# Optimization experiments

Hardware: AMD Instinct MI355X
Metric: run time of the kernel (lower is better)

Reference implementation:

```python
import jax, jax.numpy as jnp
import numpy as np

B, N, IN_DIM, HID = 8, 2048, 128, 64
LN_EPS = 1e-5
NEG_INF = -9e15
LRELU_SLOPE = 0.2


def setup_inputs() -> dict:
    key = jax.random.key(0)
    k1, k2, k3, k4, k5, k6 = jax.random.split(key, 6)
    stdv = 1.0 / np.sqrt(HID)
    adj = jax.random.randint(k1, (B, N, N), 0, 2, dtype=jnp.int32)
    # ensure self-loops so every row has at least one valid entry
    adj = adj.at[:, jnp.arange(N), jnp.arange(N)].set(1)
    return {
        "adj": adj,
        "x": jax.random.normal(k2, (B, N, IN_DIM), dtype=jnp.float32),
        "h": jax.random.normal(k3, (B, N, HID), dtype=jnp.float32),
        "X2H": jax.random.uniform(k4, (IN_DIM, 3 * HID), minval=-stdv, maxval=stdv, dtype=jnp.float32),
        "H2H": jax.random.uniform(k5, (HID, 3 * HID), minval=-stdv, maxval=stdv, dtype=jnp.float32),
        "a": jax.random.uniform(k6, (2 * HID, 1), minval=-stdv, maxval=stdv, dtype=jnp.float32),
    }


def _gated_inputs(x, h, X2H, H2H):
    gate_x = x @ X2H          # [B,N,3H]
    gate_h = h @ H2H          # [B,N,3H]
    i_r, i_i, i_n = jnp.split(gate_x, 3, axis=2)
    h_r, h_i, h_n = jnp.split(gate_h, 3, axis=2)
    resetgate = jax.nn.sigmoid(i_r + h_r)
    inputgate = jax.nn.sigmoid(i_i + h_i)
    irh = i_n + resetgate * h_n
    mu = jnp.mean(irh, axis=-1, keepdims=True)
    var = jnp.mean(jnp.square(irh - mu), axis=-1, keepdims=True)
    irh = (irh - mu) * jax.lax.rsqrt(var + LN_EPS)  # layer_norm, no affine
    newgate = jnp.tanh(irh)
    return newgate + inputgate * (h - newgate)


def reference(adj, x, h, X2H, H2H, a):
    Wh = _gated_inputs(x, h, X2H, H2H)              # [B,N,H]
    Wh1 = Wh @ a[:HID]                              # [B,N,1]
    Wh2 = Wh @ a[HID:]                              # [B,N,1]
    e = jax.nn.leaky_relu(Wh1 + jnp.swapaxes(Wh2, 1, 2), LRELU_SLOPE)  # [B,N,N]
    scores = jnp.where(adj != 0, e, jnp.float32(NEG_INF))
    attention = jax.nn.softmax(scores, axis=2)
    h_prime = attention @ Wh                        # [B,N,H]
    return (h_prime, Wh)
```

## Files before the change

kernel.cpp:

```cpp
#include <hip/hip_runtime.h>

constexpr int BB  = 8;
constexpr int NN  = 2048;
constexpr int IND = 128;
constexpr int HD  = 64;
constexpr float LN_EPS = 1e-5f;
constexpr float SLOPE  = 0.2f;

typedef _Float16 half8 __attribute__((ext_vector_type(8)));
typedef _Float16 half4 __attribute__((ext_vector_type(4)));
typedef float    f32x4 __attribute__((ext_vector_type(4)));

__device__ __forceinline__ float wave_sum(float v) {
    #pragma unroll
    for (int off = 32; off > 0; off >>= 1) v += __shfl_xor(v, off);
    return v;
}
__device__ __forceinline__ float wave_max(float v) {
    #pragma unroll
    for (int off = 32; off > 0; off >>= 1) v = fmaxf(v, __shfl_xor(v, off));
    return v;
}

__global__ __launch_bounds__(256) void k_gates(
    const float* __restrict__ x, const float* __restrict__ h,
    const float* __restrict__ X2H, const float* __restrict__ H2H,
    const float* __restrict__ a,
    float* __restrict__ Wh_out, _Float16* __restrict__ Whh2,
    float* __restrict__ Wh1, float* __restrict__ Wh2)
{
    const int lane = threadIdx.x & 63;
    const int wid  = threadIdx.x >> 6;
    const int base = (blockIdx.x * 4 + wid) * 8;

    float gx0[8] = {0}, gx1[8] = {0}, gx2[8] = {0};
    float gh0[8] = {0}, gh1[8] = {0}, gh2[8] = {0};

    for (int d4 = 0; d4 < IND; d4 += 4) {
        float w0[4], w1[4], w2[4];
        #pragma unroll
        for (int dd = 0; dd < 4; ++dd) {
            const float* wp = X2H + (size_t)(d4 + dd) * 192;
            w0[dd] = wp[lane]; w1[dd] = wp[64 + lane]; w2[dd] = wp[128 + lane];
        }
        #pragma unroll
        for (int rr = 0; rr < 8; ++rr) {
            f32x4 xv = *(const f32x4*)(x + (size_t)(base + rr) * IND + d4);
            #pragma unroll
            for (int dd = 0; dd < 4; ++dd) {
                gx0[rr] = fmaf(xv[dd], w0[dd], gx0[rr]);
                gx1[rr] = fmaf(xv[dd], w1[dd], gx1[rr]);
                gx2[rr] = fmaf(xv[dd], w2[dd], gx2[rr]);
            }
        }
    }
    for (int d4 = 0; d4 < HD; d4 += 4) {
        float w0[4], w1[4], w2[4];
        #pragma unroll
        for (int dd = 0; dd < 4; ++dd) {
            const float* wp = H2H + (size_t)(d4 + dd) * 192;
            w0[dd] = wp[lane]; w1[dd] = wp[64 + lane]; w2[dd] = wp[128 + lane];
        }
        #pragma unroll
        for (int rr = 0; rr < 8; ++rr) {
            f32x4 hv = *(const f32x4*)(h + (size_t)(base + rr) * HD + d4);
            #pragma unroll
            for (int dd = 0; dd < 4; ++dd) {
                gh0[rr] = fmaf(hv[dd], w0[dd], gh0[rr]);
                gh1[rr] = fmaf(hv[dd], w1[dd], gh1[rr]);
                gh2[rr] = fmaf(hv[dd], w2[dd], gh2[rr]);
            }
        }
    }

    const float a0 = a[lane], a1 = a[64 + lane];
    half8 p8;
    for (int rr = 0; rr < 8; ++rr) {
        const int row = base + rr;
        const float hr = h[(size_t)row * HD + lane];
        const float rg = 1.f / (1.f + __expf(-(gx0[rr] + gh0[rr])));
        const float ig = 1.f / (1.f + __expf(-(gx1[rr] + gh1[rr])));
        float irh = gx2[rr] + rg * gh2[rr];
        const float mu = wave_sum(irh) * (1.f / 64.f);
        const float dv = irh - mu;
        const float var = wave_sum(dv * dv) * (1.f / 64.f);
        const float ng = tanhf(dv * rsqrtf(var + LN_EPS));
        const float wh = ng + ig * (hr - ng);
        Wh_out[(size_t)row * HD + lane] = wh;
        p8[rr] = (_Float16)wh;
        const float d1 = wave_sum(wh * a0);
        const float d2 = wave_sum(wh * a1);
        if (lane == 0) { Wh1[row] = d1; Wh2[row] = d2; }
    }
    *(half8*)(Whh2 + ((size_t)(base >> 3) * 64 + lane) * 8) = p8;
}

constexpr int PSTR = NN + 8;

__global__ __launch_bounds__(256) void k_attn(
    const int* __restrict__ adj,
    const _Float16* __restrict__ Whh2,
    const float* __restrict__ Wh1, const float* __restrict__ Wh2,
    float* __restrict__ hp)
{
    __shared__ __align__(16) _Float16 Pbuf[16 * PSTR];
    __shared__ float redbuf[4];
    __shared__ float lsum[16];

    const int tid  = threadIdx.x;
    const int lane = tid & 63;
    const int wid  = tid >> 6;
    const int b    = blockIdx.x >> 7;
    const int i0   = (blockIdx.x & 127) * 16;

    f32x4 wv[8];
    const f32x4* __restrict__ w2v = (const f32x4*)(Wh2 + (size_t)b * NN);
    #pragma unroll
    for (int k = 0; k < 8; ++k) wv[k] = w2v[lane + 64 * k];

    float mx = -3e38f;
    #pragma unroll
    for (int k = 0; k < 8; ++k)
        mx = fmaxf(mx, fmaxf(fmaxf(wv[k][0], wv[k][1]), fmaxf(wv[k][2], wv[k][3])));
    mx = wave_max(mx);
    if (lane == 0) redbuf[wid] = mx;
    __syncthreads();
    const float M = fmaxf(fmaxf(redbuf[0], redbuf[1]), fmaxf(redbuf[2], redbuf[3]));

    const int4* __restrict__ atile = (const int4*)(adj + ((size_t)b * NN + i0) * NN);
    #pragma unroll
    for (int rr = 0; rr < 4; ++rr) {
        const int r = wid * 4 + rr;
        const float w1 = Wh1[b * NN + i0 + r];
        const float t0 = w1 + M;
        const float c  = (t0 > 0.f) ? t0 : SLOPE * t0;
        const int4* __restrict__ arow = atile + (size_t)r * (NN / 4);

        int4 av[8];
        #pragma unroll
        for (int k = 0; k < 8; ++k) av[k] = arow[lane + 64 * k];

        float sum = 0.f;
        #pragma unroll
        for (int k = 0; k < 8; ++k) {
            const int ai[4] = {av[k].x, av[k].y, av[k].z, av[k].w};
            half4 ph;
            #pragma unroll
            for (int d = 0; d < 4; ++d) {
                const float t = w1 + wv[k][d];
                const float e = (t > 0.f) ? t : SLOPE * t;
                const float p = ai[d] ? __expf(e - c) : 0.f;
                sum += p;
                ph[d] = (_Float16)p;
            }
            *(half4*)&Pbuf[r * PSTR + 4 * (lane + 64 * k)] = ph;
        }
        sum = wave_sum(sum);
        if (lane == 0) lsum[r] = sum;
    }
    __syncthreads();

    const int n0 = wid * 16;
    const int m  = lane & 15;
    const int q  = lane >> 4;
    const half8* __restrict__ Wp = (const half8*)(Whh2 + (size_t)b * NN * HD);
    const _Float16* __restrict__ prow = &Pbuf[m * PSTR];

    f32x4 acc = {0.f, 0.f, 0.f, 0.f};
    #pragma unroll 4
    for (int k0 = 0; k0 < NN; k0 += 32) {
        const half8 av = *(const half8*)(prow + k0 + q * 8);
        const half8 bv = Wp[((k0 >> 3) + q) * 64 + n0 + m];
        acc = __builtin_amdgcn_mfma_f32_16x16x32_f16(av, bv, acc, 0, 0, 0);
    }
    #pragma unroll
    for (int r2 = 0; r2 < 4; ++r2) {
        const int irow = q * 4 + r2;
        const float inv = 1.f / lsum[irow];
        hp[((size_t)b * NN + i0 + irow) * HD + n0 + m] = acc[r2] * inv;
    }
}

extern "C" void kernel_launch(void* const* d_in, const int* in_sizes, int n_in,
                              void* d_out, int out_size, void* d_ws, size_t ws_size,
                              hipStream_t stream) {
    const int*   adj = (const int*)d_in[0];
    const float* x   = (const float*)d_in[1];
    const float* h   = (const float*)d_in[2];
    const float* X2H = (const float*)d_in[3];
    const float* H2H = (const float*)d_in[4];
    const float* a   = (const float*)d_in[5];

    float* out = (float*)d_out;
    float* hp  = out;
    float* Wh  = out + (size_t)BB * NN * HD;

    float*    Wh1  = (float*)d_ws;
    float*    Wh2  = Wh1 + BB * NN;
    _Float16* Whh2 = (_Float16*)(Wh2 + BB * NN);

    k_gates<<<dim3((BB * NN) / 32), dim3(256), 0, stream>>>(
        x, h, X2H, H2H, a, Wh, Whh2, Wh1, Wh2);
    k_attn<<<dim3(BB * (NN / 16)), dim3(256), 0, stream>>>(
        adj, Whh2, Wh1, Wh2, hp);
}
```

Baseline: 259.0 us.

## Restructure attention into single-wave chunked pipeline with register-prefetched adjacency

Measured after the change: 318.0 us. 22.8% more time.

```diff
diff --git a/kernel.cpp b/kernel.cpp
--- a/kernel.cpp
+++ b/kernel.cpp
@@ -95,23 +95,23 @@
     *(half8*)(Whh2 + ((size_t)(base >> 3) * 64 + lane) * 8) = p8;
 }
 
-constexpr int PSTR = NN + 8;
-
-__global__ __launch_bounds__(256) void k_attn(
+constexpr int KC   = 256;
+constexpr int PST  = KC + 8;
+constexpr int NCHK = NN / KC;
+
+__global__ __launch_bounds__(64, 1) void k_attn(
     const int* __restrict__ adj,
     const _Float16* __restrict__ Whh2,
     const float* __restrict__ Wh1, const float* __restrict__ Wh2,
     float* __restrict__ hp)
 {
-    __shared__ __align__(16) _Float16 Pbuf[16 * PSTR];
-    __shared__ float redbuf[4];
-    __shared__ float lsum[16];
-
-    const int tid  = threadIdx.x;
-    const int lane = tid & 63;
-    const int wid  = tid >> 6;
+    __shared__ __align__(16) _Float16 Pbuf[16 * PST];
+
+    const int lane = threadIdx.x;
     const int b    = blockIdx.x >> 7;
     const int i0   = (blockIdx.x & 127) * 16;
+    const int m    = lane & 15;
+    const int q    = lane >> 4;
 
     f32x4 wv[8];
     const f32x4* __restrict__ w2v = (const f32x4*)(Wh2 + (size_t)b * NN);
@@ -122,62 +122,82 @@
     #pragma unroll
     for (int k = 0; k < 8; ++k)
         mx = fmaxf(mx, fmaxf(fmaxf(wv[k][0], wv[k][1]), fmaxf(wv[k][2], wv[k][3])));
-    mx = wave_max(mx);
-    if (lane == 0) redbuf[wid] = mx;
-    __syncthreads();
-    const float M = fmaxf(fmaxf(redbuf[0], redbuf[1]), fmaxf(redbuf[2], redbuf[3]));
-
-    const int4* __restrict__ atile = (const int4*)(adj + ((size_t)b * NN + i0) * NN);
-    #pragma unroll
-    for (int rr = 0; rr < 4; ++rr) {
-        const int r = wid * 4 + rr;
-        const float w1 = Wh1[b * NN + i0 + r];
-        const float t0 = w1 + M;
-        const float c  = (t0 > 0.f) ? t0 : SLOPE * t0;
-        const int4* __restrict__ arow = atile + (size_t)r * (NN / 4);
-
-        int4 av[8];
-        #pragma unroll
-        for (int k = 0; k < 8; ++k) av[k] = arow[lane + 64 * k];
-
-        float sum = 0.f;
-        #pragma unroll
-        for (int k = 0; k < 8; ++k) {
-            const int ai[4] = {av[k].x, av[k].y, av[k].z, av[k].w};
+    const float M = wave_max(mx);
+
+    float w1r[16], cr[16];
+    #pragma unroll
+    for (int r = 0; r < 16; ++r) {
+        w1r[r] = Wh1[b * NN + i0 + r];
+        const float t0 = w1r[r] + M;
+        cr[r] = (t0 > 0.f) ? t0 : SLOPE * t0;
+    }
+
+    const int* __restrict__ abase = adj + ((size_t)b * NN + i0) * NN;
+    const half8* __restrict__ Wp  = (const half8*)(Whh2 + (size_t)b * NN * HD);
+
+    float sacc[16];
+    #pragma unroll
+    for (int r = 0; r < 16; ++r) sacc[r] = 0.f;
+    f32x4 acc[4];
+    #pragma unroll
+    for (int cc = 0; cc < 4; ++cc) acc[cc] = (f32x4){0.f, 0.f, 0.f, 0.f};
+
+    int4 av[16];
+    #pragma unroll
+    for (int r = 0; r < 16; ++r)
+        av[r] = *(const int4*)(abase + (size_t)r * NN + lane * 4);
+
+    for (int c = 0; c < NCHK; ++c) {
+        #pragma unroll
+        for (int r = 0; r < 16; ++r) {
+            const int ai[4] = {av[r].x, av[r].y, av[r].z, av[r].w};
             half4 ph;
+            float s = 0.f;
             #pragma unroll
             for (int d = 0; d < 4; ++d) {
-                const float t = w1 + wv[k][d];
+                const float t = w1r[r] + wv[c][d];
                 const float e = (t > 0.f) ? t : SLOPE * t;
-                const float p = ai[d] ? __expf(e - c) : 0.f;
-                sum += p;
+                const float p = ai[d] ? __expf(e - cr[r]) : 0.f;
+                s += p;
                 ph[d] = (_Float16)p;
             }
-            *(half4*)&Pbuf[r * PSTR + 4 * (lane + 64 * k)] = ph;
-        }
-        sum = wave_sum(sum);
-        if (lane == 0) lsum[r] = sum;
-    }
-    __syncthreads();
-
-    const int n0 = wid * 16;
-    const int m  = lane & 15;
-    const int q  = lane >> 4;
-    const half8* __restrict__ Wp = (const half8*)(Whh2 + (size_t)b * NN * HD);
-    const _Float16* __restrict__ prow = &Pbuf[m * PSTR];
-
-    f32x4 acc = {0.f, 0.f, 0.f, 0.f};
-    #pragma unroll 4
-    for (int k0 = 0; k0 < NN; k0 += 32) {
-        const half8 av = *(const half8*)(prow + k0 + q * 8);
-        const half8 bv = Wp[((k0 >> 3) + q) * 64 + n0 + m];
-        acc = __builtin_amdgcn_mfma_f32_16x16x32_f16(av, bv, acc, 0, 0, 0);
-    }
-    #pragma unroll
-    for (int r2 = 0; r2 < 4; ++r2) {
-        const int irow = q * 4 + r2;
-        const float inv = 1.f / lsum[irow];
-        hp[((size_t)b * NN + i0 + irow) * HD + n0 + m] = acc[r2] * inv;
+            sacc[r] += s;
+            *(half4*)&Pbuf[r * PST + 4 * lane] = ph;
+        }
+        if (c + 1 < NCHK) {
+            #pragma unroll
+            for (int r = 0; r < 16; ++r)
+                av[r] = *(const int4*)(abase + (size_t)r * NN + (c + 1) * KC + lane * 4);
+        }
+        __syncthreads();
+
+        #pragma unroll
+        for (int cc = 0; cc < 4; ++cc) {
+            #pragma unroll
+            for (int k8 = 0; k8 < 8; ++k8) {
+                const half8 a8 = *(const half8*)&Pbuf[m * PST + k8 * 32 + q * 8];
+                const half8 b8 = Wp[(size_t)(c * 32 + k8 * 4 + q) * 64 + cc * 16 + m];
+                acc[cc] = __builtin_amdgcn_mfma_f32_16x16x32_f16(a8, b8, acc[cc], 0, 0, 0);
+            }
+        }
+        __syncthreads();
+    }
+
+    float linv[16];
+    #pragma unroll
+    for (int r = 0; r < 16; ++r) linv[r] = 1.f / wave_sum(sacc[r]);
+
+    #pragma unroll
+    for (int cc = 0; cc < 4; ++cc) {
+        #pragma unroll
+        for (int r2 = 0; r2 < 4; ++r2) {
+            float l = (q == 0) ? linv[r2]
+                    : (q == 1) ? linv[4 + r2]
+                    : (q == 2) ? linv[8 + r2]
+                               : linv[12 + r2];
+            const int irow = q * 4 + r2;
+            hp[((size_t)b * NN + i0 + irow) * HD + cc * 16 + m] = acc[cc][r2] * l;
+        }
     }
 }
 
@@ -201,6 +221,6 @@
 
     k_gates<<<dim3((BB * NN) / 32), dim3(256), 0, stream>>>(
         x, h, X2H, H2H, a, Wh, Whh2, Wh1, Wh2);
-    k_attn<<<dim3(BB * (NN / 16)), dim3(256), 0, stream>>>(
+    k_attn<<<dim3(BB * (NN / 16)), dim3(64), 0, stream>>>(
         adj, Whh2, Wh1, Wh2, hp);
 }
```
